# Performance work log

Hardware: AMD Instinct MI355X
Metric: run time of the kernel (lower is better)

The kernel has to match this reference:

```python
import jax, jax.numpy as jnp
import numpy as np

RADIUS = 4
SIGMA_X = 4.0
SIGMA_I = 10.0
P = 64                      # patch_size
NS = 2 * RADIUS + 1         # neighborhood_size = 9
EPS = float(np.finfo(np.float64).eps)


def _dist_weights():
    # Faithful to torch: dist varies only along the LAST window axis
    # (torch `expand` of a 1-D tensor to (9,9,9) broadcasts along dim -1).
    d = jnp.arange(1, NS + 1) - (RADIUS + 1)          # -4..4
    dist3d = jnp.broadcast_to(3 * d ** 2, (NS, NS, NS)).astype(jnp.float32)
    mask = (dist3d <= RADIUS).astype(jnp.float32)
    return (mask * jnp.exp(-dist3d / SIGMA_X ** 2)).reshape(-1)  # (729,)


_OFFSETS = jnp.asarray(
    np.stack(np.meshgrid(np.arange(NS), np.arange(NS), np.arange(NS), indexing='ij'),
             axis=-1).reshape(-1, 3), dtype=jnp.int32)            # (729, 3)


def _forward(batch, preds):
    B = batch.shape[0]
    K = preds.shape[1]
    pad = [(0, 0), (0, 0), (RADIUS, RADIUS), (RADIUS, RADIUS), (RADIUS, RADIUS)]
    pb = jnp.pad(batch, pad, constant_values=EPS)   # [B,1,P+2r,P+2r,P+2r]
    pp = jnp.pad(preds, pad, constant_values=EPS)   # [B,K,P+2r,P+2r,P+2r]
    dw = _dist_weights()

    def body(carry, od):
        off, w_o = od
        num, den = carry
        img_win = jax.lax.dynamic_slice(pb, (0, 0, off[0], off[1], off[2]),
                                        (B, 1, P, P, P))
        # Gaussian intensity affinity * spatial weight for this offset
        w = jnp.exp(-(img_win - batch) ** 2 / SIGMA_I ** 2) * w_o   # [B,1,P,P,P]
        pred_win = jax.lax.dynamic_slice(pp, (0, 0, off[0], off[1], off[2]),
                                         (B, K, P, P, P))
        return (num + w * pred_win, den + w), None

    num0 = jnp.zeros((B, K, P, P, P), batch.dtype)
    den0 = jnp.zeros((B, 1, P, P, P), batch.dtype)
    (num_map, den_map), _ = jax.lax.scan(body, (num0, den0), (_OFFSETS, dw))

    # Faithful to torch broadcasting: preds[B,1,P,P,P] * map[B,P,P,P] -> [B,B,...],
    # i.e. each sample's preds are contracted with the batch-summed maps.
    num_s = num_map.sum(axis=0)          # [K,P,P,P]
    den_s = den_map.sum(axis=0)[0]       # [P,P,P]
    numerator = jnp.einsum('bkxyz,kxyz->bk', preds, num_s)
    denominator = jnp.einsum('bkxyz,xyz->bk', preds, den_s)
    loss = (numerator + EPS) / (denominator + EPS)   # [B,K]
    return K - loss.sum(axis=1)                      # [B]


def setup_inputs() -> dict:
    key = jax.random.key(0)
    k1, k2 = jax.random.split(key)
    batch = jax.random.uniform(k1, (4, 1, P, P, P), dtype=jnp.float32)
    preds = jax.random.uniform(k2, (4, 4, P, P, P), dtype=jnp.float32)
    return {"batch": batch, "preds": preds}


def reference(batch, preds):
    return _forward(batch, preds)
```

## Files before the change

kernel.cpp:

```cpp
#include <hip/hip_runtime.h>
#include <hip/hip_fp16.h>


constexpr int Pdim = 64;
constexpr int P3   = Pdim * Pdim * Pdim;
constexpr int NREP = 16;

#define EPSF 2.2204460492503131e-16f

constexpr float WZ1   = 0.8290291181804004f;
constexpr float K2F   = 0.014426950408889634f;
constexpr float C1F   = 0.02f;
constexpr float WFULL = 81.0f * (1.0f + 2.0f * WZ1);

template<int X0, int NX, int FIRSTW>
__device__ __forceinline__ void passx_body(const float* __restrict__ Ip,
                                           const float* __restrict__ Pp,
                                           __half2* __restrict__ Uo,
                                           bool isden) {
  float w0[9], w1[9];
#pragma unroll
  for (int i = 0; i < 9; ++i) { w0[i] = 0.f; w1[i] = 0.f; }
  float s0 = 0.f, s1 = 0.f;
#pragma unroll
  for (int i = 0; i < NX; ++i) {
    const int x = X0 + i;
    float u0 = 0.f, u1 = 0.f;
    if (x < 64) {
      float I = Ip[x << 12];
      float g = exp2f(-I * I * K2F);
      float p = isden ? 1.f : Pp[x << 12];
      u0 = g * p;
      u1 = u0 * I;
    }
    const int r = i % 9;
    s0 += u0 - w0[r]; w0[r] = u0;
    s1 += u1 - w1[r]; w1[r] = u1;
    if (i >= FIRSTW) Uo[(x - 4) << 12] = __floats2half2_rn(s0, s1);
  }
}

__global__ __launch_bounds__(256)
void ncuts_passx(const float* __restrict__ batch, const float* __restrict__ preds,
                 __half2* __restrict__ U, float* __restrict__ acc) {
  const int t = threadIdx.x;
  if (blockIdx.x == 0 && blockIdx.y == 0 && blockIdx.z == 0) {
    acc[t] = 0.f; acc[t + 256] = 0.f;
  }
  const int z = t & 63, ys = t >> 6;
  const int y = blockIdx.x * 4 + ys;
  const int pair = blockIdx.y;
  const int b = pair / 5, c = pair - 5 * b;
  const bool isden = (c == 4);
  const int lin = (y << 6) + z;
  const float* Ip = batch + b * P3 + lin;
  const float* Pp = isden ? Ip : preds + (b * 4 + c) * P3 + lin;
  __half2* Uo = U + pair * P3 + lin;
  if (blockIdx.z == 0) passx_body< 0, 36, 4>(Ip, Pp, Uo, isden);
  else                 passx_body<28, 40, 8>(Ip, Pp, Uo, isden);
}

template<int Y0, int NY, int FIRSTW>
__device__ __forceinline__ void passyz_body(const __half2* __restrict__ src,
                                            __half2* __restrict__ dst, int z) {
  float w0[9], w1[9];
#pragma unroll
  for (int i = 0; i < 9; ++i) { w0[i] = 0.f; w1[i] = 0.f; }
  float s0 = 0.f, s1 = 0.f;
#pragma unroll
  for (int i = 0; i < NY; ++i) {
    const int y = Y0 + i;
    float u0 = 0.f, u1 = 0.f;
    if (y < 64) {
      float2 u = __half22float2(src[y << 6]);
      u0 = u.x; u1 = u.y;
    }
    const int r = i % 9;
    s0 += u0 - w0[r]; w0[r] = u0;
    s1 += u1 - w1[r]; w1[r] = u1;
    if (i >= FIRSTW) {
      float up0 = __shfl_up(s0, 1, 64),   up1 = __shfl_up(s1, 1, 64);
      float dn0 = __shfl_down(s0, 1, 64), dn1 = __shfl_down(s1, 1, 64);
      if (z == 0)  { up0 = 0.f; up1 = 0.f; }
      if (z == 63) { dn0 = 0.f; dn1 = 0.f; }
      float v0 = __builtin_fmaf(WZ1, up0 + dn0, s0);
      float v1 = __builtin_fmaf(WZ1, up1 + dn1, s1);
      dst[(y - 4) << 6] = __floats2half2_rn(v0, v1);
    }
  }
}

__global__ __launch_bounds__(256)
void ncuts_passyz(const __half2* __restrict__ U, __half2* __restrict__ V) {
  const int t = threadIdx.x;
  const int z = t & 63, xs = t >> 6;
  const int x = blockIdx.x * 4 + xs;
  const int pair = blockIdx.y;
  const __half2* src = U + pair * P3 + (x << 12) + z;
  __half2* dst = V + pair * P3 + (x << 12) + z;
  if (blockIdx.z == 0) passyz_body< 0, 36, 4>(src, dst, z);
  else                 passyz_body<28, 40, 8>(src, dst, z);
}

__global__ __launch_bounds__(256)
void ncuts_contract(const float* __restrict__ batch, const float* __restrict__ preds,
                    const __half2* __restrict__ V, float* __restrict__ acc) {
  __shared__ float red[4][32];
  const int t = threadIdx.x;
  float pn[16], pd[16];
#pragma unroll
  for (int i = 0; i < 16; ++i) { pn[i] = 0.f; pd[i] = 0.f; }

#pragma unroll 1
  for (int it = 0; it < 2; ++it) {
    const int v = blockIdx.x * 512 + it * 256 + t;
    const int z = v & 63, y = (v >> 6) & 63, x = v >> 12;

    float a0[4], a1[4], gsum = 0.f;
#pragma unroll
    for (int b = 0; b < 4; ++b) {
      float I = batch[b * P3 + v];
      float g = exp2f(-I * I * K2F);
      a0[b] = g; a1[b] = g * I * C1F; gsum += g;
    }

    float ns[4] = {0.f, 0.f, 0.f, 0.f};
    float ds = 0.f;
#pragma unroll
    for (int b = 0; b < 4; ++b) {
#pragma unroll
      for (int c = 0; c < 5; ++c) {
        float2 u = __half22float2(V[(b * 5 + c) * P3 + v]);
        float zc = __builtin_fmaf(a0[b], u.x, a1[b] * u.y);
        if (c < 4) ns[c] += zc;
        else       ds    += zc;
      }
    }
    float cx = (float)(9 - max(0, 4 - x) - max(0, x - 59));
    float cy = (float)(9 - max(0, 4 - y) - max(0, y - 59));
    float cz = 1.f + WZ1 * (float)((int)(z > 0) + (int)(z < 63));
    ds = __builtin_fmaf(gsum, WFULL - cx * cy * cz, ds);

#pragma unroll
    for (int b = 0; b < 4; ++b) {
#pragma unroll
      for (int k = 0; k < 4; ++k) {
        float p = preds[(b * 4 + k) * P3 + v];
        pn[b * 4 + k] = __builtin_fmaf(p, ns[k], pn[b * 4 + k]);
        pd[b * 4 + k] = __builtin_fmaf(p, ds,    pd[b * 4 + k]);
      }
    }
  }

#pragma unroll
  for (int i = 0; i < 16; ++i) {
#pragma unroll
    for (int off = 32; off > 0; off >>= 1) {
      pn[i] += __shfl_down(pn[i], off, 64);
      pd[i] += __shfl_down(pd[i], off, 64);
    }
  }
  const int wave = t >> 6, lane = t & 63;
  if (lane == 0) {
#pragma unroll
    for (int i = 0; i < 16; ++i) { red[wave][i] = pn[i]; red[wave][16 + i] = pd[i]; }
  }
  __syncthreads();
  if (t < 32) {
    float s = red[0][t] + red[1][t] + red[2][t] + red[3][t];
    atomicAdd(&acc[(blockIdx.x & (NREP - 1)) * 32 + t], s);
  }
}

__global__ void ncuts_final(const float* __restrict__ acc, float* __restrict__ out) {
  __shared__ float loss[16];
  int t = threadIdx.x;
  if (t < 16) {
    float n = 0.f, d = 0.f;
    for (int r = 0; r < NREP; ++r) { n += acc[r * 32 + t]; d += acc[r * 32 + 16 + t]; }
    loss[t] = (n + EPSF) / (d + EPSF);
  }
  __syncthreads();
  if (t < 4) {
    float s = loss[t * 4] + loss[t * 4 + 1] + loss[t * 4 + 2] + loss[t * 4 + 3];
    out[t] = 4.0f - s;
  }
}

constexpr int Rxy = 4;
constexpr int TX = 8, TY = 8;
constexpr int ZLEN = 2;
constexpr int RGX = 16, RGY = 16, RGZ = 10;
constexpr int YP = 17, ZP = 11;

__global__ __launch_bounds__(256, 2)
void ncuts_main(const float* __restrict__ batch, const float* __restrict__ preds,
                float* __restrict__ acc) {
  __shared__ float  sB[RGX][YP][ZP];
  __shared__ float4 sP[RGX][YP][ZP];
  __shared__ float  red[4][32];

  const int t = threadIdx.x;
  const int tx = t & 7, ty = (t >> 3) & 7, tzt = t >> 6;
  const int bx0 = blockIdx.x * TX, by0 = blockIdx.y * TY, bz0 = blockIdx.z * 8;
  const int x = bx0 + tx, y = by0 + ty, z0 = bz0 + tzt * ZLEN;
  const int zc = tzt * ZLEN;

  float  den[ZLEN];
  float4 num[ZLEN];
#pragma unroll
  for (int j = 0; j < ZLEN; ++j) { den[j] = 0.f; num[j] = make_float4(0.f, 0.f, 0.f, 0.f); }

  const float C1 = -0.014426950408889634f;
  const float LWZ1 = -0.27050531991668065f;

  for (int b = 0; b < 4; ++b) {
    __syncthreads();
    for (int idx = t; idx < RGX * RGY * RGZ; idx += 256) {
      int rz = idx % RGZ, rq = idx / RGZ, ry = rq % RGY, rx = rq / RGY;
      int gx = bx0 + rx - Rxy, gy = by0 + ry - Rxy, gz = bz0 + rz - 1;
      bool in = ((unsigned)gx < 64u) & ((unsigned)gy < 64u) & ((unsigned)gz < 64u);
      float v = EPSF; float4 pv = make_float4(EPSF, EPSF, EPSF, EPSF);
      if (in) {
        int gi = (gx * Pdim + gy) * Pdim + gz;
        v = batch[b * P3 + gi];
        const float* pp = preds + b * 4 * P3 + gi;
        pv.x = pp[0]; pv.y = pp[P3]; pv.z = pp[2 * P3]; pv.w = pp[3 * P3];
      }
      sB[rx][ry][rz] = v; sP[rx][ry][rz] = pv;
    }
    __syncthreads();

    float I0[ZLEN];
#pragma unroll
    for (int j = 0; j < ZLEN; ++j) I0[j] = sB[tx + Rxy][ty + Rxy][zc + 1 + j];

#pragma unroll 1
    for (int dy = 0; dy < 9; ++dy) {
#pragma unroll 3
      for (int dx = 0; dx < 9; ++dx) {
        const float*  cb = &sB[tx + dx][ty + dy][zc];
        const float4* cp = &sP[tx + dx][ty + dy][zc];
        float colB[ZLEN + 2]; float4 colP[ZLEN + 2];
#pragma unroll
        for (int j = 0; j < ZLEN + 2; ++j) { colB[j] = cb[j]; colP[j] = cp[j]; }
#pragma unroll
        for (int j = 0; j < ZLEN; ++j) {
#pragma unroll
          for (int dz = 0; dz < 3; ++dz) {
            float d = colB[j + dz] - I0[j];
            float arg = __builtin_fmaf(d * d, C1, (dz == 1) ? 0.f : LWZ1);
            float w = exp2f(arg);
            den[j] += w;
            float4 p = colP[j + dz];
            num[j].x = __builtin_fmaf(w, p.x, num[j].x);
            num[j].y = __builtin_fmaf(w, p.y, num[j].y);
            num[j].z = __builtin_fmaf(w, p.z, num[j].z);
            num[j].w = __builtin_fmaf(w, p.w, num[j].w);
          }
        }
      }
    }
  }

  float pn[16], pd[16];
#pragma unroll
  for (int i = 0; i < 16; ++i) { pn[i] = 0.f; pd[i] = 0.f; }
#pragma unroll
  for (int b = 0; b < 4; ++b) {
#pragma unroll
    for (int j = 0; j < ZLEN; ++j) {
      const float* pp = preds + b * 4 * P3 + ((x * Pdim + y) * Pdim + z0 + j);
      float nsv[4] = {num[j].x, num[j].y, num[j].z, num[j].w};
#pragma unroll
      for (int k = 0; k < 4; ++k) {
        float pv = pp[k * P3];
        pn[b * 4 + k] = __builtin_fmaf(pv, nsv[k], pn[b * 4 + k]);
        pd[b * 4 + k] = __builtin_fmaf(pv, den[j], pd[b * 4 + k]);
      }
    }
  }
#pragma unroll
  for (int i = 0; i < 16; ++i) {
#pragma unroll
    for (int off = 32; off > 0; off >>= 1) {
      pn[i] += __shfl_down(pn[i], off, 64);
      pd[i] += __shfl_down(pd[i], off, 64);
    }
  }
  const int wave = t >> 6, lane = t & 63;
  if (lane == 0) {
#pragma unroll
    for (int i = 0; i < 16; ++i) { red[wave][i] = pn[i]; red[wave][16 + i] = pd[i]; }
  }
  __syncthreads();
  if (t < 32) {
    float s = red[0][t] + red[1][t] + red[2][t] + red[3][t];
    int bid = blockIdx.x + 8 * (blockIdx.y + 8 * (int)blockIdx.z);
    atomicAdd(&acc[(bid & (NREP - 1)) * 32 + t], s);
  }
}

__global__ void ncuts_zero(float* __restrict__ acc) {
  int t = threadIdx.x;
  if (t < NREP * 32) acc[t] = 0.f;
}

extern "C" void kernel_launch(void* const* d_in, const int* in_sizes, int n_in,
                              void* d_out, int out_size, void* d_ws, size_t ws_size,
                              hipStream_t stream) {
  const float* batch = (const float*)d_in[0];
  const float* preds = (const float*)d_in[1];
  float* out = (float*)d_out;

  const size_t fbytes = (size_t)20 * P3 * sizeof(__half2);
  const size_t need   = 2 * fbytes + 8192;
  if (ws_size >= need) {
    __half2* U   = (__half2*)((char*)d_ws + 256);
    __half2* V   = (__half2*)((char*)d_ws + 256 + fbytes);
    float*   acc = (float*)((char*)d_ws + 512 + 2 * fbytes);
    hipLaunchKernelGGL(ncuts_passx,  dim3(16, 20, 2), dim3(256), 0, stream,
                       batch, preds, U, acc);
    hipLaunchKernelGGL(ncuts_passyz, dim3(16, 20, 2), dim3(256), 0, stream, U, V);
    hipLaunchKernelGGL(ncuts_contract, dim3(512), dim3(256), 0, stream,
                       batch, preds, V, acc);
    hipLaunchKernelGGL(ncuts_final, dim3(1), dim3(64), 0, stream, acc, out);
  } else {
    float* acc = (float*)d_ws;
    hipLaunchKernelGGL(ncuts_zero, dim3(1), dim3(512), 0, stream, acc);
    hipLaunchKernelGGL(ncuts_main, dim3(8, 8, 8), dim3(256), 0, stream,
                       batch, preds, acc);
    hipLaunchKernelGGL(ncuts_final, dim3(1), dim3(64), 0, stream, acc, out);
  }
}
```

Measured before the change: 97.80 us.

## Fuse x and y/z box-filter passes into one kernel using shared-memory y sums

Merges the separate x-pass and yz-pass kernels into one kernel. Each block stages the per-voxel Gaussian weights for a y-tile plus halo in shared memory, sums nine y-neighbours there, runs a sliding window along x in registers, and does the z stencil with wave shuffles. This removes the intermediate U buffer and its global write and read, plus one kernel launch. In exchange it adds two __syncthreads per x step, redundant halo loads in y, and fp16 accumulation of the y sums, which lowers precision.

```diff
diff --git a/kernel.cpp b/kernel.cpp
--- a/kernel.cpp
+++ b/kernel.cpp
@@ -13,93 +13,116 @@
 constexpr float C1F   = 0.02f;
 constexpr float WFULL = 81.0f * (1.0f + 2.0f * WZ1);
 
-template<int X0, int NX, int FIRSTW>
-__device__ __forceinline__ void passx_body(const float* __restrict__ Ip,
-                                           const float* __restrict__ Pp,
-                                           __half2* __restrict__ Uo,
-                                           bool isden) {
-  float w0[9], w1[9];
-#pragma unroll
-  for (int i = 0; i < 9; ++i) { w0[i] = 0.f; w1[i] = 0.f; }
+template<int X0, int FIRSTW, bool TAIL>
+__device__ __forceinline__ void fused_body(const float* __restrict__ Ib,
+                                           const float* __restrict__ Pb,
+                                           __half2* __restrict__ Vo,
+                                           __half2* __restrict__ S,
+                                           int w, int z, int ybase, bool isden) {
+  int  gy[3]; bool oky[3];
+#pragma unroll
+  for (int j = 0; j < 3; ++j) {
+    gy[j]  = ybase + w + 4 * j;
+    oky[j] = ((unsigned)gy[j] < 64u);
+  }
+  const int soff0 = z * 13 + w;
+
+  float f0[9], f1[9];
+#pragma unroll
+  for (int i = 0; i < 9; ++i) { f0[i] = 0.f; f1[i] = 0.f; }
   float s0 = 0.f, s1 = 0.f;
-#pragma unroll
-  for (int i = 0; i < NX; ++i) {
-    const int x = X0 + i;
-    float u0 = 0.f, u1 = 0.f;
-    if (x < 64) {
-      float I = Ip[x << 12];
-      float g = exp2f(-I * I * K2F);
-      float p = isden ? 1.f : Pp[x << 12];
-      u0 = g * p;
-      u1 = u0 * I;
-    }
-    const int r = i % 9;
-    s0 += u0 - w0[r]; w0[r] = u0;
-    s1 += u1 - w1[r]; w1[r] = u1;
-    if (i >= FIRSTW) Uo[(x - 4) << 12] = __floats2half2_rn(s0, s1);
-  }
-}
-
-__global__ __launch_bounds__(256)
-void ncuts_passx(const float* __restrict__ batch, const float* __restrict__ preds,
-                 __half2* __restrict__ U, float* __restrict__ acc) {
-  const int t = threadIdx.x;
-  if (blockIdx.x == 0 && blockIdx.y == 0 && blockIdx.z == 0) {
-    acc[t] = 0.f; acc[t + 256] = 0.f;
-  }
-  const int z = t & 63, ys = t >> 6;
-  const int y = blockIdx.x * 4 + ys;
-  const int pair = blockIdx.y;
-  const int b = pair / 5, c = pair - 5 * b;
-  const bool isden = (c == 4);
-  const int lin = (y << 6) + z;
-  const float* Ip = batch + b * P3 + lin;
-  const float* Pp = isden ? Ip : preds + (b * 4 + c) * P3 + lin;
-  __half2* Uo = U + pair * P3 + lin;
-  if (blockIdx.z == 0) passx_body< 0, 36, 4>(Ip, Pp, Uo, isden);
-  else                 passx_body<28, 40, 8>(Ip, Pp, Uo, isden);
-}
-
-template<int Y0, int NY, int FIRSTW>
-__device__ __forceinline__ void passyz_body(const __half2* __restrict__ src,
-                                            __half2* __restrict__ dst, int z) {
-  float w0[9], w1[9];
-#pragma unroll
-  for (int i = 0; i < 9; ++i) { w0[i] = 0.f; w1[i] = 0.f; }
-  float s0 = 0.f, s1 = 0.f;
-#pragma unroll
-  for (int i = 0; i < NY; ++i) {
-    const int y = Y0 + i;
-    float u0 = 0.f, u1 = 0.f;
-    if (y < 64) {
-      float2 u = __half22float2(src[y << 6]);
-      u0 = u.x; u1 = u.y;
-    }
-    const int r = i % 9;
-    s0 += u0 - w0[r]; w0[r] = u0;
-    s1 += u1 - w1[r]; w1[r] = u1;
-    if (i >= FIRSTW) {
+
+  float LI[3][3], LP[3][3];
+#pragma unroll
+  for (int sidx = 0; sidx < 2; ++sidx) {
+#pragma unroll
+    for (int j = 0; j < 3; ++j) {
+      if (oky[j]) {
+        const int a = ((X0 + sidx) << 12) + (gy[j] << 6) + z;
+        LI[sidx][j] = Ib[a];
+        LP[sidx][j] = isden ? 1.f : Pb[a];
+      } else { LI[sidx][j] = 0.f; LP[sidx][j] = 0.f; }
+    }
+  }
+
+  for (int o = 0; o < 2; ++o) {
+#pragma unroll
+    for (int ii = 0; ii < 18; ++ii) {
+      const int i   = o * 18 + ii;
+      const int x   = X0 + i;
+      const int cur = ii % 3;
+      const int nxt = (ii + 2) % 3;
+      __syncthreads();
+#pragma unroll
+      for (int j = 0; j < 3; ++j) {
+        float I  = LI[cur][j], p = LP[cur][j];
+        float g  = exp2f(-I * I * K2F);
+        float F0 = g * p;
+        S[soff0 + 4 * j] = __floats2half2_rn(F0, F0 * I);
+      }
+      if (i + 2 < 36) {
+#pragma unroll
+        for (int j = 0; j < 3; ++j) {
+          if (oky[j]) {
+            const int a = ((x + 2) << 12) + (gy[j] << 6) + z;
+            LI[nxt][j] = Ib[a];
+            LP[nxt][j] = isden ? 1.f : Pb[a];
+          } else { LI[nxt][j] = 0.f; LP[nxt][j] = 0.f; }
+        }
+      }
+      __syncthreads();
+      __half2 a2 = S[soff0];
+#pragma unroll
+      for (int dy = 1; dy < 9; ++dy) a2 = __hadd2(a2, S[soff0 + dy]);
+      float2 yb = __half22float2(a2);
+      const int r = ii % 9;
+      s0 += yb.x - f0[r]; f0[r] = yb.x;
+      s1 += yb.y - f1[r]; f1[r] = yb.y;
+      if (i >= FIRSTW) {
+        float up0 = __shfl_up(s0, 1, 64),   up1 = __shfl_up(s1, 1, 64);
+        float dn0 = __shfl_down(s0, 1, 64), dn1 = __shfl_down(s1, 1, 64);
+        if (z == 0)  { up0 = 0.f; up1 = 0.f; }
+        if (z == 63) { dn0 = 0.f; dn1 = 0.f; }
+        float v0 = __builtin_fmaf(WZ1, up0 + dn0, s0);
+        float v1 = __builtin_fmaf(WZ1, up1 + dn1, s1);
+        Vo[(x - 4) << 12] = __floats2half2_rn(v0, v1);
+      }
+    }
+  }
+  if (TAIL) {
+#pragma unroll
+    for (int k = 0; k < 4; ++k) {
+      const int x = X0 + 36 + k;
+      s0 -= f0[k]; s1 -= f1[k];
       float up0 = __shfl_up(s0, 1, 64),   up1 = __shfl_up(s1, 1, 64);
       float dn0 = __shfl_down(s0, 1, 64), dn1 = __shfl_down(s1, 1, 64);
       if (z == 0)  { up0 = 0.f; up1 = 0.f; }
       if (z == 63) { dn0 = 0.f; dn1 = 0.f; }
       float v0 = __builtin_fmaf(WZ1, up0 + dn0, s0);
       float v1 = __builtin_fmaf(WZ1, up1 + dn1, s1);
-      dst[(y - 4) << 6] = __floats2half2_rn(v0, v1);
+      Vo[(x - 4) << 12] = __floats2half2_rn(v0, v1);
     }
   }
 }
 
 __global__ __launch_bounds__(256)
-void ncuts_passyz(const __half2* __restrict__ U, __half2* __restrict__ V) {
+void ncuts_fused(const float* __restrict__ batch, const float* __restrict__ preds,
+                 __half2* __restrict__ V, float* __restrict__ acc) {
+  __shared__ __half2 S[832];
   const int t = threadIdx.x;
-  const int z = t & 63, xs = t >> 6;
-  const int x = blockIdx.x * 4 + xs;
+  if (blockIdx.x == 0 && blockIdx.y == 0 && blockIdx.z == 0) {
+    acc[t] = 0.f; acc[t + 256] = 0.f;
+  }
+  const int w = t >> 6, z = t & 63;
   const int pair = blockIdx.y;
-  const __half2* src = U + pair * P3 + (x << 12) + z;
-  __half2* dst = V + pair * P3 + (x << 12) + z;
-  if (blockIdx.z == 0) passyz_body< 0, 36, 4>(src, dst, z);
-  else                 passyz_body<28, 40, 8>(src, dst, z);
+  const int b = pair / 5, c = pair - 5 * b;
+  const bool isden = (c == 4);
+  const int y0 = blockIdx.x * 4;
+  const float* Ib = batch + b * P3;
+  const float* Pb = isden ? Ib : preds + (b * 4 + c) * P3;
+  __half2* Vo = V + pair * P3 + ((y0 + w) << 6) + z;
+  if (blockIdx.z == 0) fused_body< 0, 4, false>(Ib, Pb, Vo, S, w, z, y0 - 4, isden);
+  else                 fused_body<28, 8, true >(Ib, Pb, Vo, S, w, z, y0 - 4, isden);
 }
 
 __global__ __launch_bounds__(256)
@@ -314,14 +337,12 @@
   float* out = (float*)d_out;
 
   const size_t fbytes = (size_t)20 * P3 * sizeof(__half2);
-  const size_t need   = 2 * fbytes + 8192;
+  const size_t need   = fbytes + 8192;
   if (ws_size >= need) {
-    __half2* U   = (__half2*)((char*)d_ws + 256);
-    __half2* V   = (__half2*)((char*)d_ws + 256 + fbytes);
-    float*   acc = (float*)((char*)d_ws + 512 + 2 * fbytes);
-    hipLaunchKernelGGL(ncuts_passx,  dim3(16, 20, 2), dim3(256), 0, stream,
-                       batch, preds, U, acc);
-    hipLaunchKernelGGL(ncuts_passyz, dim3(16, 20, 2), dim3(256), 0, stream, U, V);
+    __half2* V   = (__half2*)((char*)d_ws + 256);
+    float*   acc = (float*)((char*)d_ws + 256 + fbytes);
+    hipLaunchKernelGGL(ncuts_fused, dim3(16, 20, 2), dim3(256), 0, stream,
+                       batch, preds, V, acc);
     hipLaunchKernelGGL(ncuts_contract, dim3(512), dim3(256), 0, stream,
                        batch, preds, V, acc);
     hipLaunchKernelGGL(ncuts_final, dim3(1), dim3(64), 0, stream, acc, out);
```

Measured after the change: 99.12 us. Within noise of the previous version (+1.4%).
